# Performance work log

Measured on AMD Instinct MI355X. Metric: run time of the kernel, lower is better.

The kernel has to match this reference:

```python
import jax, jax.numpy as jnp
import numpy as np

ALPHABET = 8
DIM = 128
SEQ_LEN = 8192
POWER_ITERS = 200


def setup_inputs() -> dict:
    key = jax.random.key(0)
    k1, k2, k3 = jax.random.split(key, 3)
    return {
        "Kraus_op_re": jax.random.uniform(k1, (ALPHABET, DIM, DIM), dtype=jnp.float32),
        "Kraus_op_im": jax.random.uniform(k2, (ALPHABET, DIM, DIM), dtype=jnp.float32),
        "sequence": jax.random.randint(k3, (SEQ_LEN,), 0, ALPHABET),
    }


def _leading_eig(K):
    # K: [A, d, d] complex. Power iteration on the transfer map and its adjoint.
    d = K.shape[-1]
    Kc = K.conj()

    def body_r(rhor, _):
        # rhov = sum_x K_x @ rhor @ K_x^H
        rhov = jnp.einsum("aij,jk,alk->il", K, rhor, Kc)
        mu = jnp.trace(rhov).real
        return rhov / mu.astype(rhov.dtype), None

    rhor, _ = jax.lax.scan(body_r, jnp.eye(d, dtype=K.dtype) / d, None, length=POWER_ITERS)

    def body_l(carry, _):
        rhol, _ = carry
        # rhov = sum_x K_x^H @ rhol @ K_x
        rhov = jnp.einsum("aji,jk,akl->il", Kc, rhol, K)
        mu = jnp.trace(rhov).real
        return (rhov / mu.astype(rhov.dtype), mu), None

    (rhol, mu), _ = jax.lax.scan(
        body_l, (jnp.eye(d, dtype=K.dtype), jnp.asarray(1.0, jnp.float32)), None, length=POWER_ITERS
    )
    return rhor, rhol, mu


def reference(Kraus_op_re, Kraus_op_im, sequence):
    K = Kraus_op_re.astype(jnp.complex64) + 1j * Kraus_op_im.astype(jnp.complex64)
    rhor, rhol, lam = _leading_eig(K)
    # normalize so that trace(rho @ rhol) == 1
    rho0 = rhor / jnp.trace(rhor @ rhol).real.astype(rhor.dtype)
    Kn = K / jnp.sqrt(lam).astype(K.dtype)  # Kraus ops rescaled by sqrt(leading eigenvalue)
    L = sequence.shape[0]

    def step(carry, inp):
        rho, logp = carry
        i, x = inp
        Kx = Kn[x]
        rho = Kx @ rho @ Kx.conj().T
        px = jnp.where(i == L - 1, jnp.trace(rho @ rhol).real, jnp.trace(rho).real)
        logp = logp - jnp.log2(px)
        rho = rho / px.astype(rho.dtype)
        return (rho, logp), None

    (_, log_p), _ = jax.lax.scan(
        step, (rho0, jnp.asarray(0.0, jnp.float32)), (jnp.arange(L), sequence)
    )
    return log_p[None]  # matches torch.tensor([0.0]) accumulator shape (1,)
```

## Files before the change

### kernel.cpp

```cpp
#include <hip/hip_runtime.h>

typedef unsigned int u32;
typedef unsigned short u16;
typedef __attribute__((ext_vector_type(4))) float f32x4;
typedef __attribute__((ext_vector_type(8))) short s16x8;
typedef __attribute__((ext_vector_type(4))) u32 u32x4;

#define DIMN 128
#define MATN (DIMN*DIMN)
#define NA 8
#define LSEQ 8192
#define NTOK (LSEQ/2)
#define PITERS 4
#define S1SH 5
#define S2SH 6
#define CHSH 7
#define P2SH 8

struct WS {
  u16 *Kb, *P2b, *rho, *nodes0, *nodes1, *rootR, *rootI;
  int *tok, *E0, *E1, *Eroot;
  float *trbuf;
  float *out;
  int G, g;
};

__device__ __forceinline__ u16 f2bf(float x){
  u32 u = __float_as_uint(x);
  u32 r = (u + 0x7FFFu + ((u >> 16) & 1u)) >> 16;
  return (u16)r;
}
__device__ __forceinline__ float bf2f(u16 u){ return __uint_as_float(((u32)u) << 16); }
__device__ __forceinline__ u32 cvtpk(float lo, float hi){
  u32 r; asm("v_cvt_pk_bf16_f32 %0, %1, %2" : "=v"(r) : "v"(lo), "v"(hi)); return r;
}
__device__ __forceinline__ s16x8 negi(s16x8 v){
  return __builtin_bit_cast(s16x8, __builtin_bit_cast(u32x4, v) ^ 0x80008000u);
}
__device__ __forceinline__ int swz16(int maj, int b){
  return maj*256 + (((((b >> 4) + maj*5) & 15) << 4) | (b & 15));
}
__device__ __forceinline__ void cfma2(float2& c, float2 a, float2 b){
  c.x = fmaf(a.x, b.x, c.x); c.x = fmaf(-a.y, b.y, c.x);
  c.y = fmaf(a.x, b.y, c.y); c.y = fmaf(a.y, b.x, c.y);
}
template<int CA, int CB>
__device__ __forceinline__ void cmfma(s16x8 a_r, s16x8 a_i, s16x8 b_r, s16x8 b_i,
                                      f32x4& qr, f32x4& qi){
  s16x8 t1 = (CA ^ CB) ? a_i : negi(a_i);
  s16x8 t2 = CB ? negi(a_r) : a_r;
  s16x8 t3 = CA ? negi(a_i) : a_i;
  qr = __builtin_amdgcn_mfma_f32_16x16x32_bf16(a_r, b_r, qr, 0,0,0);
  qr = __builtin_amdgcn_mfma_f32_16x16x32_bf16(t1,  b_i, qr, 0,0,0);
  qi = __builtin_amdgcn_mfma_f32_16x16x32_bf16(t2,  b_i, qi, 0,0,0);
  qi = __builtin_amdgcn_mfma_f32_16x16x32_bf16(t3,  b_r, qi, 0,0,0);
}

__global__ __launch_bounds__(256) void k_init(const int* seq, WS w){
  int gid = blockIdx.x*256 + threadIdx.x;
  int gsz = gridDim.x*256;
  for (int i = gid; i < NTOK; i += gsz)
    w.tok[i] = seq[2*i+1]*NA + seq[2*i];
  for (int i = gid; i < 4*MATN; i += gsz){
    int plane = (i >> 14) & 1, rem = i & (MATN-1);
    u16 v = (plane == 0 && (rem >> 7) == (rem & 127)) ? f2bf(1.f) : (u16)0;
    w.rho[i] = v;
  }
  if (gid < 32) w.trbuf[gid] = 0.f;
}

__global__ __launch_bounds__(256) void k_kb(const float* Kre, const float* Kim, WS w){
  __shared__ u16 Lr[32][36], Li[32][36];
  int blk = blockIdx.x, x = blk >> 4, tile = blk & 15;
  int row0 = (tile>>2)*32, col0 = (tile&3)*32;
  int t = threadIdx.x;
  { int r = t>>3, cch = t&7;
    size_t off = (size_t)x*MATN + (size_t)(row0+r)*128 + col0 + cch*4;
    float4 vr = *(const float4*)(Kre + off);
    float4 vi = *(const float4*)(Kim + off);
    Lr[r][cch*4+0] = f2bf(vr.x); Lr[r][cch*4+1] = f2bf(vr.y);
    Lr[r][cch*4+2] = f2bf(vr.z); Lr[r][cch*4+3] = f2bf(vr.w);
    Li[r][cch*4+0] = f2bf(vi.x); Li[r][cch*4+1] = f2bf(vi.y);
    Li[r][cch*4+2] = f2bf(vi.z); Li[r][cch*4+3] = f2bf(vi.w);
  }
  __syncthreads();
  u16* b = w.Kb + (size_t)x*4*MATN;
  { int r = t>>3, cch = t&7;
    *(uint2*)&b[(row0+r)*128 + col0 + cch*4]        = *(uint2*)&Lr[r][cch*4];
    *(uint2*)&b[MATN + (row0+r)*128 + col0 + cch*4] = *(uint2*)&Li[r][cch*4];
  }
  { int c = t>>3, rch = t&7;
    ushort4 vr, vi;
    vr.x = Lr[rch*4+0][c]; vr.y = Lr[rch*4+1][c];
    vr.z = Lr[rch*4+2][c]; vr.w = Lr[rch*4+3][c];
    vi.x = Li[rch*4+0][c]; vi.y = Li[rch*4+1][c];
    vi.z = Li[rch*4+2][c]; vi.w = Li[rch*4+3][c];
    *(ushort4*)&b[2*MATN + (col0+c)*128 + row0 + rch*4] = vr;
    *(ushort4*)&b[3*MATN + (col0+c)*128 + row0 + rch*4] = vi;
  }
}

__global__ __launch_bounds__(256) void k_p2(const float* Kre, const float* Kim, WS w){
  __shared__ float2 As[16][33], Bs[16][33];
  int blk = blockIdx.x, mat = blk >> 4, tile = blk & 15;
  int a = mat >> 3, b = mat & 7;
  int row0 = (tile>>2)*32, col0 = (tile&3)*32;
  int t = threadIdx.x, ti = t & 15, tk = t >> 4;
  float2 acc[4] = {{0,0},{0,0},{0,0},{0,0}};
  for (int k0 = 0; k0 < 128; k0 += 16){
    { int r = t >> 4, kk = t & 15;
      size_t i0 = (size_t)a*MATN + (size_t)(row0+r)*DIMN + k0+kk;
      size_t i1 = i0 + 16*DIMN;
      As[kk][r]    = make_float2(Kre[i0], Kim[i0]);
      As[kk][r+16] = make_float2(Kre[i1], Kim[i1]); }
    { int kk = t >> 5, c = t & 31;
      size_t i0 = (size_t)b*MATN + (size_t)(k0+kk)*DIMN + col0+c;
      size_t i1 = i0 + 8*DIMN;
      Bs[kk][c]   = make_float2(Kre[i0], Kim[i0]);
      Bs[kk+8][c] = make_float2(Kre[i1], Kim[i1]); }
    __syncthreads();
    #pragma unroll
    for (int jj = 0; jj < 16; jj++){
      float2 a0 = As[jj][ti], a1 = As[jj][ti+16];
      float2 b0 = Bs[jj][tk], b1 = Bs[jj][tk+16];
      cfma2(acc[0], a0, b0); cfma2(acc[1], a0, b1);
      cfma2(acc[2], a1, b0); cfma2(acc[3], a1, b1);
    }
    __syncthreads();
  }
  u16* Lr = (u16*)As; u16* Li = (u16*)Bs;
  const float sc = 1.f/(1<<P2SH);
  Lr[ti*36+tk]         = f2bf(acc[0].x*sc); Li[ti*36+tk]         = f2bf(acc[0].y*sc);
  Lr[ti*36+tk+16]      = f2bf(acc[1].x*sc); Li[ti*36+tk+16]      = f2bf(acc[1].y*sc);
  Lr[(ti+16)*36+tk]    = f2bf(acc[2].x*sc); Li[(ti+16)*36+tk]    = f2bf(acc[2].y*sc);
  Lr[(ti+16)*36+tk+16] = f2bf(acc[3].x*sc); Li[(ti+16)*36+tk+16] = f2bf(acc[3].y*sc);
  __syncthreads();
  u16* base = w.P2b + (size_t)mat*4*MATN;
  { int r = t>>3, cch = t&7;
    *(uint2*)&base[(row0+r)*128 + col0 + cch*4]        = *(uint2*)&Lr[r*36 + cch*4];
    *(uint2*)&base[MATN + (row0+r)*128 + col0 + cch*4] = *(uint2*)&Li[r*36 + cch*4];
  }
  { int c = t>>3, rch = t&7;
    ushort4 vr, vi;
    vr.x = Lr[(rch*4+0)*36 + c]; vr.y = Lr[(rch*4+1)*36 + c];
    vr.z = Lr[(rch*4+2)*36 + c]; vr.w = Lr[(rch*4+3)*36 + c];
    vi.x = Li[(rch*4+0)*36 + c]; vi.y = Li[(rch*4+1)*36 + c];
    vi.z = Li[(rch*4+2)*36 + c]; vi.w = Li[(rch*4+3)*36 + c];
    *(ushort4*)&base[2*MATN + (col0+c)*128 + row0 + rch*4] = vr;
    *(ushort4*)&base[3*MATN + (col0+c)*128 + row0 + rch*4] = vi;
  }
}

__device__ __forceinline__ void ccompute(const u16* Ar, const u16* Ai,
    const char* Pr, const char* Pi, f32x4 (&qr)[2][4], f32x4 (&qi)[2][4], int t){
  int wv = t>>6, lane = t&63, l15 = lane&15, hi = lane>>4;
  int wr = (wv>>1)*32, wc = (wv&1)*64;
  #pragma unroll
  for (int m=0;m<2;m++)
    #pragma unroll
    for (int n=0;n<4;n++){ qr[m][n] = (f32x4){0,0,0,0}; qi[m][n] = (f32x4){0,0,0,0}; }
  #pragma unroll
  for (int kk = 0; kk < 4; kk++){
    int kb = kk*32 + hi*8;
    s16x8 a_r[2], a_i[2];
    #pragma unroll
    for (int m=0;m<2;m++){
      int r = wr + m*16 + l15;
      a_r[m] = *(const s16x8*)(Ar + r*128 + kb);
      a_i[m] = *(const s16x8*)(Ai + r*128 + kb);
    }
    #pragma unroll
    for (int n=0;n<4;n++){
      int c = wc + n*16 + l15;
      int o = swz16(c, kb*2);
      s16x8 b_r = *(const s16x8*)(Pr + o);
      s16x8 b_i = *(const s16x8*)(Pi + o);
      #pragma unroll
      for (int m=0;m<2;m++)
        cmfma<0,0>(a_r[m], a_i[m], b_r, b_i, qr[m][n], qi[m][n]);
    }
  }
}
__device__ __forceinline__ void pwrite8(char* Pr, char* Pi,
    f32x4 (&qr)[2][4], f32x4 (&qi)[2][4], float sc, int t){
  int wv = t>>6, lane = t&63, l15 = lane&15, hi = lane>>4;
  int wr = (wv>>1)*32, wc = (wv&1)*64;
  #pragma unroll
  for (int m=0;m<2;m++)
    #pragma unroll
    for (int n=0;n<4;n++){
      int c = wc + n*16 + l15, r0 = wr + m*16 + hi*4;
      uint2 pr, pi;
      pr.x = cvtpk(qr[m][n][0]*sc, qr[m][n][1]*sc);
      pr.y = cvtpk(qr[m][n][2]*sc, qr[m][n][3]*sc);
      pi.x = cvtpk(qi[m][n][0]*sc, qi[m][n][1]*sc);
      pi.y = cvtpk(qi[m][n][2]*sc, qi[m][n][3]*sc);
      int o = swz16(c, r0*2);
      *(uint2*)(Pr + o) = pr;
      *(uint2*)(Pi + o) = pi;
    }
}
__device__ __forceinline__ int renorm8(char* Pr, char* Pi,
    f32x4 (&qr)[2][4], f32x4 (&qi)[2][4], int t){
  int wv = t>>6, lane = t&63;
  float lm = 0.f;
  #pragma unroll
  for (int m=0;m<2;m++)
    #pragma unroll
    for (int n=0;n<4;n++)
      #pragma unroll
      for (int j=0;j<4;j++)
        lm = fmaxf(lm, fmaxf(fabsf(qr[m][n][j]), fabsf(qi[m][n][j])));
  #pragma unroll
  for (int o = 32; o > 0; o >>= 1) lm = fmaxf(lm, __shfl_xor(lm, o, 64));
  if (lane == 0) ((float*)Pr)[wv] = lm;
  __syncthreads();
  float mx = 0.f;
  #pragma unroll
  for (int i = 0; i < 8; i++) mx = fmaxf(mx, ((float*)Pr)[i]);
  int e = 0; if (mx > 0.f) frexpf(mx, &e);
  __syncthreads();
  pwrite8(Pr, Pi, qr, qi, ldexpf(1.f, -e), t);
  return e;
}
__device__ __forceinline__ void stage_cols(const u16* gr, const u16* gi,
                                           char* Pr, char* Pi, int t){
  #pragma unroll
  for (int i = 0; i < 4; i++){
    int chunk = t + i*512;
    int c = chunk >> 4, rr = chunk & 15;
    int o = swz16(c, rr*16);
    *(uint4*)(Pr + o) = *(const uint4*)(gr + c*128 + rr*8);
    *(uint4*)(Pi + o) = *(const uint4*)(gi + c*128 + rr*8);
  }
}
__device__ __forceinline__ void write_node(u16* dr, u16* di,
    const char* Pr, const char* Pi, bool rowLayout, int t){
  if (!rowLayout){
    #pragma unroll
    for (int i = 0; i < 4; i++){
      int chunk = t + i*512;
      int c = chunk >> 4, rr = chunk & 15;
      int o = swz16(c, rr*16);
      *(uint4*)(dr + c*128 + rr*8) = *(const uint4*)(Pr + o);
      *(uint4*)(di + c*128 + rr*8) = *(const uint4*)(Pi + o);
    }
  } else {
    for (int idx = t; idx < MATN; idx += 512){
      int r = idx >> 7, c = idx & 127;
      int o = swz16(c, r*2);
      dr[idx] = *(const u16*)(Pr + o);
      di[idx] = *(const u16*)(Pi + o);
    }
  }
}

__global__ __launch_bounds__(512,2) void k_chain(WS w){
  __shared__ __align__(16) char Pr[32768];
  __shared__ __align__(16) char Pi[32768];
  int p = blockIdx.x, t = threadIdx.x;
  int tok0 = w.tok[p*w.g];
  const u16* b0 = w.P2b + (size_t)tok0*4*MATN;
  stage_cols(b0 + 2*MATN, b0 + 3*MATN, Pr, Pi, t);
  f32x4 qr[2][4], qi[2][4];
  int eLast = 0;
  for (int s = 1; s < w.g; s++){
    const u16* tb = w.P2b + (size_t)w.tok[p*w.g + s]*4*MATN;
    __syncthreads();
    ccompute(tb, tb + MATN, Pr, Pi, qr, qi, t);
    __syncthreads();
    if (s < w.g-1) pwrite8(Pr, Pi, qr, qi, 1.f/(1<<CHSH), t);
    else eLast = renorm8(Pr, Pi, qr, qi, t);
  }
  __syncthreads();
  u16* slot = w.nodes0 + (size_t)p*2*MATN;
  write_node(slot, slot + MATN, Pr, Pi, (p & 3) != 0, t);
  if (t == 0) w.E0[p] = P2SH*w.g + CHSH*(w.g-2) + eLast;
}

__global__ __launch_bounds__(512,2) void k_level(WS w, int srcIs0, int radix,
                                                 int mask, int isRoot){
  __shared__ __align__(16) char Pr[32768];
  __shared__ __align__(16) char Pi[32768];
  int p = blockIdx.x, t = threadIdx.x;
  const u16* src = srcIs0 ? w.nodes0 : w.nodes1;
  u16* dst       = srcIs0 ? w.nodes1 : w.nodes0;
  const int* Es  = srcIs0 ? w.E0 : w.E1;
  int* Ed        = srcIs0 ? w.E1 : w.E0;
  const u16* B = src + (size_t)(radix*p)*2*MATN;
  stage_cols(B, B + MATN, Pr, Pi, t);
  int E = 0;
  for (int j = 0; j < radix; j++) E += Es[radix*p + j];
  f32x4 qr[2][4], qi[2][4];
  for (int j = 1; j < radix; j++){
    const u16* A = src + (size_t)(radix*p + j)*2*MATN;
    __syncthreads();
    ccompute(A, A + MATN, Pr, Pi, qr, qi, t);
    __syncthreads();
    E += renorm8(Pr, Pi, qr, qi, t);
  }
  __syncthreads();
  u16* slot = dst + (size_t)p*2*MATN;
  write_node(slot, slot + MATN, Pr, Pi, ((p & mask) != 0) || isRoot, t);
  if (t == 0) Ed[p] = E;
}

__global__ __launch_bounds__(512,1) void k_pow(WS w, int par){
  __shared__ __align__(16) char Rr[32768];
  __shared__ __align__(16) char Ri[32768];
  __shared__ __align__(16) char Yr[32768];
  __shared__ __align__(16) char Yi[32768];
  int b = blockIdx.x, side = b >> 3, rb = b & 7;
  int t = threadIdx.x, wv = t>>6, lane = t&63, l15 = lane&15, hi = lane>>4;
  const u16* rhoS = w.rho + (size_t)((par*2 + side)*2)*MATN;
  stage_cols(rhoS, rhoS + MATN, Rr, Ri, t);
  __syncthreads();
  {
    int x = wv;
    const u16* Ab = w.Kb + (size_t)(x*4 + (side ? 2 : 0))*MATN;
    const u16* Ar = Ab; const u16* Ai = Ab + MATN;
    f32x4 q1r[8], q1i[8];
    #pragma unroll
    for (int n=0;n<8;n++){ q1r[n] = (f32x4){0,0,0,0}; q1i[n] = (f32x4){0,0,0,0}; }
    #pragma unroll
    for (int kk = 0; kk < 4; kk++){
      int kb = kk*32 + hi*8;
      int r = rb*16 + l15;
      s16x8 a_r = *(const s16x8*)(Ar + r*128 + kb);
      s16x8 a_i = *(const s16x8*)(Ai + r*128 + kb);
      #pragma unroll
      for (int n=0;n<8;n++){
        int c = n*16 + l15;
        int o = swz16(c, kb*2);
        s16x8 b_r = *(const s16x8*)(Rr + o);
        s16x8 b_i = *(const s16x8*)(Ri + o);
        if (side == 0) cmfma<0,0>(a_r, a_i, b_r, b_i, q1r[n], q1i[n]);
        else           cmfma<1,0>(a_r, a_i, b_r, b_i, q1r[n], q1i[n]);
      }
    }
    const float sc = 1.f/(1<<S1SH);
    #pragma unroll
    for (int n=0;n<8;n++)
      #pragma unroll
      for (int q=0;q<4;q++){
        int lr = hi*4 + q, c = n*16 + l15;
        *(u16*)(Yr + x*4096 + swz16(lr, c*2)) = f2bf(q1r[n][q]*sc);
        *(u16*)(Yi + x*4096 + swz16(lr, c*2)) = f2bf(q1i[n][q]*sc);
      }
  }
  __syncthreads();
  {
    int c0 = wv*16, c = c0 + l15;
    f32x4 q2r = {0,0,0,0}, q2i = {0,0,0,0};
    #pragma unroll 2
    for (int x = 0; x < 8; x++){
      const u16* Bb = w.Kb + (size_t)(x*4 + (side ? 2 : 0))*MATN;
      const u16* Br = Bb; const u16* Bi = Bb + MATN;
      #pragma unroll
      for (int kk = 0; kk < 4; kk++){
        int kb = kk*32 + hi*8;
        s16x8 a_r = *(const s16x8*)(Yr + x*4096 + swz16(l15, kb*2));
        s16x8 a_i = *(const s16x8*)(Yi + x*4096 + swz16(l15, kb*2));
        s16x8 b_r = *(const s16x8*)(Br + c*128 + kb);
        s16x8 b_i = *(const s16x8*)(Bi + c*128 + kb);
        if (side == 0) cmfma<0,1>(a_r, a_i, b_r, b_i, q2r, q2i);
        else           cmfma<0,0>(a_r, a_i, b_r, b_i, q2r, q2i);
      }
    }
    const float sc = 1.f/(1<<S2SH);
    u16* Dr = w.rho + (size_t)(((par^1)*2 + side)*2)*MATN;
    u16* Di = Dr + MATN;
    int r0g = rb*16 + hi*4;
    uint2 pr, pi;
    pr.x = cvtpk(q2r[0]*sc, q2r[1]*sc); pr.y = cvtpk(q2r[2]*sc, q2r[3]*sc);
    pi.x = cvtpk(q2i[0]*sc, q2i[1]*sc); pi.y = cvtpk(q2i[2]*sc, q2i[3]*sc);
    *(uint2*)(Dr + c*128 + r0g) = pr;
    *(uint2*)(Di + c*128 + r0g) = pi;
    if (side == 1 && wv == rb){
      float tr = 0.f;
      #pragma unroll
      for (int q=0;q<4;q++) if (hi*4 + q == l15) tr += q2r[q]*sc;
      #pragma unroll
      for (int o = 32; o > 0; o >>= 1) tr += __shfl_xor(tr, o, 64);
      if (lane == 0) w.trbuf[par*16 + 8 + rb] = tr;
    }
  }
}

__global__ __launch_bounds__(512) void k_epi(WS w){
  __shared__ __align__(16) char T1r[32768];
  __shared__ __align__(16) char T1i[32768];
  int t = threadIdx.x, wv = t>>6, lane = t&63, l15 = lane&15, hi = lane>>4;
  int wr = (wv>>2)*64, wc = (wv&3)*32;
  f32x4 qr[4][2], qi[4][2];
  const u16* Ar = w.rho;
  const u16* Ai = Ar + MATN;
  #pragma unroll
  for (int m=0;m<4;m++)
    #pragma unroll
    for (int n=0;n<2;n++){ qr[m][n] = (f32x4){0,0,0,0}; qi[m][n] = (f32x4){0,0,0,0}; }
  #pragma unroll
  for (int kk = 0; kk < 4; kk++){
    int kb = kk*32 + hi*8;
    #pragma unroll
    for (int m=0;m<4;m++){
      int r = wr + m*16 + l15;
      s16x8 a_r = *(const s16x8*)(Ar + r*128 + kb);
      s16x8 a_i = *(const s16x8*)(Ai + r*128 + kb);
      #pragma unroll
      for (int n=0;n<2;n++){
        int c = wc + n*16 + l15;
        s16x8 b_r = *(const s16x8*)(w.rootR + c*128 + kb);
        s16x8 b_i = *(const s16x8*)(w.rootI + c*128 + kb);
        cmfma<0,0>(a_r, a_i, b_r, b_i, qr[m][n], qi[m][n]);
      }
    }
  }
  {
    const float sc = 1.f/(1<<CHSH);
    #pragma unroll
    for (int m=0;m<4;m++)
      #pragma unroll
      for (int n=0;n<2;n++){
        int c = wc + n*16 + l15, r0 = wr + m*16 + hi*4;
        uint2 pr, pi;
        pr.x = cvtpk(qr[m][n][0]*sc, qr[m][n][1]*sc);
        pr.y = cvtpk(qr[m][n][2]*sc, qr[m][n][3]*sc);
        pi.x = cvtpk(qi[m][n][0]*sc, qi[m][n][1]*sc);
        pi.y = cvtpk(qi[m][n][2]*sc, qi[m][n][3]*sc);
        int o = swz16(c, r0*2);
        *(uint2*)(T1r + o) = pr;
        *(uint2*)(T1i + o) = pi;
      }
  }
  __syncthreads();
  #pragma unroll
  for (int m=0;m<4;m++)
    #pragma unroll
    for (int n=0;n<2;n++){ qr[m][n] = (f32x4){0,0,0,0}; qi[m][n] = (f32x4){0,0,0,0}; }
  #pragma unroll
  for (int kk = 0; kk < 4; kk++){
    int kb = kk*32 + hi*8;
    #pragma unroll
    for (int m=0;m<4;m++){
      int r = wr + m*16 + l15;
      int o = swz16(r, kb*2);
      s16x8 a_r = *(const s16x8*)(T1r + o);
      s16x8 a_i = *(const s16x8*)(T1i + o);
      #pragma unroll
      for (int n=0;n<2;n++){
        int c = wc + n*16 + l15;
        s16x8 b_r = *(const s16x8*)(w.rootR + c*128 + kb);
        s16x8 b_i = *(const s16x8*)(w.rootI + c*128 + kb);
        cmfma<0,1>(a_r, a_i, b_r, b_i, qr[m][n], qi[m][n]);
      }
    }
  }
  __syncthreads();
  double* red = (double*)T1r;
  const u16* rlr = w.rho + (size_t)2*MATN;
  const u16* rli = rlr + MATN;
  double a1 = 0.0;
  #pragma unroll
  for (int m=0;m<4;m++)
    #pragma unroll
    for (int n=0;n<2;n++){
      int c = wc + n*16 + l15, r0 = wr + m*16 + hi*4;
      #pragma unroll
      for (int q=0;q<4;q++){
        int r = r0 + q;
        float lr = bf2f(rlr[r*128 + c]), li = bf2f(rli[r*128 + c]);
        a1 += (double)qr[m][n][q]*lr - (double)qi[m][n][q]*li;
      }
    }
  red[t] = a1; __syncthreads();
  for (int o = 256; o > 0; o >>= 1){ if (t < o) red[t] += red[t+o]; __syncthreads(); }
  double that = red[0]; __syncthreads();
  const u16* rrr = w.rho;
  const u16* rri = rrr + MATN;
  double a2 = 0.0;
  for (int idx = t; idx < MATN; idx += 512){
    int c = idx >> 7, r = idx & 127;
    float ar_ = bf2f(rrr[idx]), ai_ = bf2f(rri[idx]);
    float lr  = bf2f(rlr[r*128 + c]), li = bf2f(rli[r*128 + c]);
    a2 += (double)ar_*lr - (double)ai_*li;
  }
  red[t] = a2; __syncthreads();
  for (int o = 256; o > 0; o >>= 1){ if (t < o) red[t] += red[t+o]; __syncthreads(); }
  double trrl = red[0];
  if (t == 0){
    double T0 = 0.0, T1s = 0.0;
    for (int s = 0; s < 8; s++){ T0 += w.trbuf[8+s]; T1s += w.trbuf[16+8+s]; }
    double lam = ldexp(T1s / T0, S1SH + S2SH);
    double logp = (double)LSEQ * log2(lam) - 2.0*(double)w.Eroot[0] - (double)CHSH
                  - log2(fmax(that, 1e-300)) + log2(fmax(trrl, 1e-300));
    w.out[0] = (float)logp;
  }
}

static inline size_t aln256(size_t x){ return (x + 255) & ~(size_t)255; }

extern "C" void kernel_launch(void* const* d_in, const int* in_sizes, int n_in,
                              void* d_out, int out_size, void* d_ws, size_t ws_size,
                              hipStream_t stream){
  const float* Kre = (const float*)d_in[0];
  const float* Kim = (const float*)d_in[1];
  const int*   seq = (const int*)d_in[2];

  size_t fixedBytes = aln256((size_t)NA*4*MATN*2) + aln256((size_t)64*4*MATN*2)
                    + aln256((size_t)8*MATN*2) + aln256(NTOK*4)
                    + 2*aln256(512*4) + aln256(32*4);
  size_t need512 = fixedBytes + aln256((size_t)512*2*MATN*2) + aln256((size_t)128*2*MATN*2);
  int G = (ws_size >= need512) ? 512 : 256;
  int g = NTOK / G;

  WS w{};
  char* p = (char*)d_ws;
  auto take = [&](size_t bytes)->char*{ char* r = p; p += aln256(bytes); return r; };
  w.Kb    = (u16*)take((size_t)NA*4*MATN*2);
  w.P2b   = (u16*)take((size_t)64*4*MATN*2);
  w.rho   = (u16*)take((size_t)8*MATN*2);
  w.nodes0= (u16*)take((size_t)G*2*MATN*2);
  w.nodes1= (u16*)take((size_t)(G/4)*2*MATN*2);
  w.tok   = (int*)take(NTOK*4);
  w.E0    = (int*)take(512*4);
  w.E1    = (int*)take(512*4);
  w.trbuf = (float*)take(32*4);
  w.G = G; w.g = g;
  w.out = (float*)d_out;

  struct Lv { int blocks, srcIs0, radix, mask, isRoot; };
  Lv lv512[5] = { {128,1,4,3,0},{32,0,4,3,0},{8,1,4,3,0},{2,0,4,1,0},{1,1,2,0,1} };
  Lv lv256[4] = { {64,1,4,3,0},{16,0,4,3,0},{4,1,4,3,0},{1,0,4,0,1} };
  Lv* lv = (G == 512) ? lv512 : lv256;
  int nlv = (G == 512) ? 5 : 4;
  if (lv[nlv-1].srcIs0){ w.rootR = w.nodes1; w.Eroot = w.E1; }
  else                 { w.rootR = w.nodes0; w.Eroot = w.E0; }
  w.rootI = w.rootR + MATN;

  hipLaunchKernelGGL(k_init, dim3(64), dim3(256), 0, stream, seq, w);
  hipLaunchKernelGGL(k_kb, dim3(NA*16), dim3(256), 0, stream, Kre, Kim, w);
  hipLaunchKernelGGL(k_p2, dim3(64*16), dim3(256), 0, stream, Kre, Kim, w);
  hipLaunchKernelGGL(k_chain, dim3(G), dim3(512), 0, stream, w);
  for (int l = 0; l < nlv; l++)
    hipLaunchKernelGGL(k_level, dim3(lv[l].blocks), dim3(512), 0, stream, w,
                       lv[l].srcIs0, lv[l].radix, lv[l].mask, lv[l].isRoot);
  for (int k = 0; k < PITERS; k++)
    hipLaunchKernelGGL(k_pow, dim3(16), dim3(512), 0, stream, w, k & 1);
  hipLaunchKernelGGL(k_epi, dim3(1), dim3(512), 0, stream, w);
}
```

Baseline: 328.3 us.

## Double-buffer LDS in chain/level kernels, prefetch A operands into registers, fix grid

```diff
diff --git a/kernel.cpp b/kernel.cpp
--- a/kernel.cpp
+++ b/kernel.cpp
@@ -16,13 +16,14 @@
 #define S2SH 6
 #define CHSH 7
 #define P2SH 8
+#define GCH 256
+#define GLG 16
 
 struct WS {
   u16 *Kb, *P2b, *rho, *nodes0, *nodes1, *rootR, *rootI;
   int *tok, *E0, *E1, *Eroot;
   float *trbuf;
   float *out;
-  int G, g;
 };
 
 __device__ __forceinline__ u16 f2bf(float x){
@@ -56,20 +57,8 @@
   qi = __builtin_amdgcn_mfma_f32_16x16x32_bf16(t3,  b_r, qi, 0,0,0);
 }
 
-__global__ __launch_bounds__(256) void k_init(const int* seq, WS w){
-  int gid = blockIdx.x*256 + threadIdx.x;
-  int gsz = gridDim.x*256;
-  for (int i = gid; i < NTOK; i += gsz)
-    w.tok[i] = seq[2*i+1]*NA + seq[2*i];
-  for (int i = gid; i < 4*MATN; i += gsz){
-    int plane = (i >> 14) & 1, rem = i & (MATN-1);
-    u16 v = (plane == 0 && (rem >> 7) == (rem & 127)) ? f2bf(1.f) : (u16)0;
-    w.rho[i] = v;
-  }
-  if (gid < 32) w.trbuf[gid] = 0.f;
-}
-
-__global__ __launch_bounds__(256) void k_kb(const float* Kre, const float* Kim, WS w){
+__global__ __launch_bounds__(256) void k_kbinit(const float* Kre, const float* Kim,
+                                                const int* seq, WS w){
   __shared__ u16 Lr[32][36], Li[32][36];
   int blk = blockIdx.x, x = blk >> 4, tile = blk & 15;
   int row0 = (tile>>2)*32, col0 = (tile&3)*32;
@@ -98,6 +87,15 @@
     *(ushort4*)&b[2*MATN + (col0+c)*128 + row0 + rch*4] = vr;
     *(ushort4*)&b[3*MATN + (col0+c)*128 + row0 + rch*4] = vi;
   }
+  int gid = blockIdx.x*256 + t, gsz = gridDim.x*256;
+  for (int i = gid; i < NTOK; i += gsz)
+    w.tok[i] = seq[2*i+1]*NA + seq[2*i];
+  for (int i = gid; i < 4*MATN; i += gsz){
+    int plane = (i >> 14) & 1, rem = i & (MATN-1);
+    u16 v = (plane == 0 && (rem >> 7) == (rem & 127)) ? f2bf(1.f) : (u16)0;
+    w.rho[i] = v;
+  }
+  if (gid < 32) w.trbuf[gid] = 0.f;
 }
 
 __global__ __launch_bounds__(256) void k_p2(const float* Kre, const float* Kim, WS w){
@@ -151,24 +149,29 @@
   }
 }
 
-__device__ __forceinline__ void ccompute(const u16* Ar, const u16* Ai,
-    const char* Pr, const char* Pi, f32x4 (&qr)[2][4], f32x4 (&qi)[2][4], int t){
-  int wv = t>>6, lane = t&63, l15 = lane&15, hi = lane>>4;
-  int wr = (wv>>1)*32, wc = (wv&1)*64;
-  #pragma unroll
-  for (int m=0;m<2;m++)
-    #pragma unroll
-    for (int n=0;n<4;n++){ qr[m][n] = (f32x4){0,0,0,0}; qi[m][n] = (f32x4){0,0,0,0}; }
+__device__ __forceinline__ void loadA(const u16* Ar, const u16* Ai,
+    int wr, int l15, int hi, s16x8 (&fr)[4][2], s16x8 (&fi)[4][2]){
   #pragma unroll
   for (int kk = 0; kk < 4; kk++){
     int kb = kk*32 + hi*8;
-    s16x8 a_r[2], a_i[2];
-    #pragma unroll
-    for (int m=0;m<2;m++){
+    #pragma unroll
+    for (int m = 0; m < 2; m++){
       int r = wr + m*16 + l15;
-      a_r[m] = *(const s16x8*)(Ar + r*128 + kb);
-      a_i[m] = *(const s16x8*)(Ai + r*128 + kb);
-    }
+      fr[kk][m] = *(const s16x8*)(Ar + r*128 + kb);
+      fi[kk][m] = *(const s16x8*)(Ai + r*128 + kb);
+    }
+  }
+}
+__device__ __forceinline__ void ccomputeR(const s16x8 (&fr)[4][2], const s16x8 (&fi)[4][2],
+    const char* Pr, const char* Pi, f32x4 (&qr)[2][4], f32x4 (&qi)[2][4],
+    int wc, int l15, int hi){
+  #pragma unroll
+  for (int m=0;m<2;m++)
+    #pragma unroll
+    for (int n=0;n<4;n++){ qr[m][n] = (f32x4){0,0,0,0}; qi[m][n] = (f32x4){0,0,0,0}; }
+  #pragma unroll
+  for (int kk = 0; kk < 4; kk++){
+    int kb = kk*32 + hi*8;
     #pragma unroll
     for (int n=0;n<4;n++){
       int c = wc + n*16 + l15;
@@ -177,11 +180,11 @@
       s16x8 b_i = *(const s16x8*)(Pi + o);
       #pragma unroll
       for (int m=0;m<2;m++)
-        cmfma<0,0>(a_r[m], a_i[m], b_r, b_i, qr[m][n], qi[m][n]);
-    }
-  }
-}
-__device__ __forceinline__ void pwrite8(char* Pr, char* Pi,
+        cmfma<0,0>(fr[kk][m], fi[kk][m], b_r, b_i, qr[m][n], qi[m][n]);
+    }
+  }
+}
+__device__ __forceinline__ void pwrite16(char* Pr, char* Pi,
     f32x4 (&qr)[2][4], f32x4 (&qi)[2][4], float sc, int t){
   int wv = t>>6, lane = t&63, l15 = lane&15, hi = lane>>4;
   int wr = (wv>>1)*32, wc = (wv&1)*64;
@@ -200,7 +203,7 @@
       *(uint2*)(Pi + o) = pi;
     }
 }
-__device__ __forceinline__ int renorm8(char* Pr, char* Pi,
+__device__ __forceinline__ int renorm_to(char* Pr, char* Pi, float* red,
     f32x4 (&qr)[2][4], f32x4 (&qi)[2][4], int t){
   int wv = t>>6, lane = t&63;
   float lm = 0.f;
@@ -213,18 +216,17 @@
         lm = fmaxf(lm, fmaxf(fabsf(qr[m][n][j]), fabsf(qi[m][n][j])));
   #pragma unroll
   for (int o = 32; o > 0; o >>= 1) lm = fmaxf(lm, __shfl_xor(lm, o, 64));
-  if (lane == 0) ((float*)Pr)[wv] = lm;
+  if (lane == 0) red[wv] = lm;
   __syncthreads();
   float mx = 0.f;
   #pragma unroll
-  for (int i = 0; i < 8; i++) mx = fmaxf(mx, ((float*)Pr)[i]);
+  for (int i = 0; i < 8; i++) mx = fmaxf(mx, red[i]);
   int e = 0; if (mx > 0.f) frexpf(mx, &e);
-  __syncthreads();
-  pwrite8(Pr, Pi, qr, qi, ldexpf(1.f, -e), t);
+  pwrite16(Pr, Pi, qr, qi, ldexpf(1.f, -e), t);
   return e;
 }
-__device__ __forceinline__ void stage_cols(const u16* gr, const u16* gi,
-                                           char* Pr, char* Pi, int t){
+__device__ __forceinline__ void stage_cols16(const u16* gr, const u16* gi,
+                                             char* Pr, char* Pi, int t){
   #pragma unroll
   for (int i = 0; i < 4; i++){
     int chunk = t + i*512;
@@ -234,7 +236,7 @@
     *(uint4*)(Pi + o) = *(const uint4*)(gi + c*128 + rr*8);
   }
 }
-__device__ __forceinline__ void write_node(u16* dr, u16* di,
+__device__ __forceinline__ void write_node16(u16* dr, u16* di,
     const char* Pr, const char* Pi, bool rowLayout, int t){
   if (!rowLayout){
     #pragma unroll
@@ -255,53 +257,93 @@
   }
 }
 
-__global__ __launch_bounds__(512,2) void k_chain(WS w){
-  __shared__ __align__(16) char Pr[32768];
-  __shared__ __align__(16) char Pi[32768];
+__global__ __launch_bounds__(512,1) void k_chain(WS w){
+  __shared__ __align__(16) char P0r[32768];
+  __shared__ __align__(16) char P0i[32768];
+  __shared__ __align__(16) char P1r[32768];
+  __shared__ __align__(16) char P1i[32768];
+  __shared__ float red[8];
   int p = blockIdx.x, t = threadIdx.x;
-  int tok0 = w.tok[p*w.g];
+  int wv = t>>6, lane = t&63, l15 = lane&15, hi = lane>>4;
+  int wr = (wv>>1)*32, wc = (wv&1)*64;
+  char *PrC = P0r, *PiC = P0i, *PrN = P1r, *PiN = P1i;
+  int tok0 = w.tok[p*GLG];
   const u16* b0 = w.P2b + (size_t)tok0*4*MATN;
-  stage_cols(b0 + 2*MATN, b0 + 3*MATN, Pr, Pi, t);
+  stage_cols16(b0 + 2*MATN, b0 + 3*MATN, PrC, PiC, t);
+  s16x8 A1r[4][2], A1i[4][2], A2r[4][2], A2i[4][2];
+  { const u16* tb = w.P2b + (size_t)w.tok[p*GLG + 1]*4*MATN;
+    loadA(tb, tb + MATN, wr, l15, hi, A1r, A1i); }
   f32x4 qr[2][4], qi[2][4];
   int eLast = 0;
-  for (int s = 1; s < w.g; s++){
-    const u16* tb = w.P2b + (size_t)w.tok[p*w.g + s]*4*MATN;
+  __syncthreads();
+  #pragma unroll 1
+  for (int s = 1; s < GLG; s += 2){
+    if (s+1 < GLG){
+      const u16* tb = w.P2b + (size_t)w.tok[p*GLG + s+1]*4*MATN;
+      loadA(tb, tb + MATN, wr, l15, hi, A2r, A2i);
+    }
+    ccomputeR(A1r, A1i, PrC, PiC, qr, qi, wc, l15, hi);
+    if (s < GLG-1) pwrite16(PrN, PiN, qr, qi, 1.f/(1<<CHSH), t);
+    else eLast = renorm_to(PrN, PiN, red, qr, qi, t);
     __syncthreads();
-    ccompute(tb, tb + MATN, Pr, Pi, qr, qi, t);
-    __syncthreads();
-    if (s < w.g-1) pwrite8(Pr, Pi, qr, qi, 1.f/(1<<CHSH), t);
-    else eLast = renorm8(Pr, Pi, qr, qi, t);
-  }
-  __syncthreads();
+    { char* x = PrC; PrC = PrN; PrN = x; x = PiC; PiC = PiN; PiN = x; }
+    if (s+1 < GLG){
+      if (s+2 < GLG){
+        const u16* tb = w.P2b + (size_t)w.tok[p*GLG + s+2]*4*MATN;
+        loadA(tb, tb + MATN, wr, l15, hi, A1r, A1i);
+      }
+      ccomputeR(A2r, A2i, PrC, PiC, qr, qi, wc, l15, hi);
+      if (s+1 < GLG-1) pwrite16(PrN, PiN, qr, qi, 1.f/(1<<CHSH), t);
+      else eLast = renorm_to(PrN, PiN, red, qr, qi, t);
+      __syncthreads();
+      { char* x = PrC; PrC = PrN; PrN = x; x = PiC; PiC = PiN; PiN = x; }
+    }
+  }
   u16* slot = w.nodes0 + (size_t)p*2*MATN;
-  write_node(slot, slot + MATN, Pr, Pi, (p & 3) != 0, t);
-  if (t == 0) w.E0[p] = P2SH*w.g + CHSH*(w.g-2) + eLast;
-}
-
-__global__ __launch_bounds__(512,2) void k_level(WS w, int srcIs0, int radix,
-                                                 int mask, int isRoot){
-  __shared__ __align__(16) char Pr[32768];
-  __shared__ __align__(16) char Pi[32768];
+  write_node16(slot, slot + MATN, PrC, PiC, (p & 3) != 0, t);
+  if (t == 0) w.E0[p] = P2SH*GLG + CHSH*(GLG-2) + eLast;
+}
+
+__global__ __launch_bounds__(512,1) void k_level(WS w, int srcIs0, int isRoot){
+  __shared__ __align__(16) char P0r[32768];
+  __shared__ __align__(16) char P0i[32768];
+  __shared__ __align__(16) char P1r[32768];
+  __shared__ __align__(16) char P1i[32768];
+  __shared__ float red[8];
   int p = blockIdx.x, t = threadIdx.x;
+  int wv = t>>6, lane = t&63, l15 = lane&15, hi = lane>>4;
+  int wr = (wv>>1)*32, wc = (wv&1)*64;
+  char *PrC = P0r, *PiC = P0i, *PrN = P1r, *PiN = P1i;
   const u16* src = srcIs0 ? w.nodes0 : w.nodes1;
   u16* dst       = srcIs0 ? w.nodes1 : w.nodes0;
   const int* Es  = srcIs0 ? w.E0 : w.E1;
   int* Ed        = srcIs0 ? w.E1 : w.E0;
-  const u16* B = src + (size_t)(radix*p)*2*MATN;
-  stage_cols(B, B + MATN, Pr, Pi, t);
-  int E = 0;
-  for (int j = 0; j < radix; j++) E += Es[radix*p + j];
+  const u16* B = src + (size_t)(4*p)*2*MATN;
+  stage_cols16(B, B + MATN, PrC, PiC, t);
+  s16x8 A1r[4][2], A1i[4][2], A2r[4][2], A2i[4][2];
+  { const u16* A = src + (size_t)(4*p+1)*2*MATN;
+    loadA(A, A + MATN, wr, l15, hi, A1r, A1i); }
+  int E = Es[4*p] + Es[4*p+1] + Es[4*p+2] + Es[4*p+3];
   f32x4 qr[2][4], qi[2][4];
-  for (int j = 1; j < radix; j++){
-    const u16* A = src + (size_t)(radix*p + j)*2*MATN;
-    __syncthreads();
-    ccompute(A, A + MATN, Pr, Pi, qr, qi, t);
-    __syncthreads();
-    E += renorm8(Pr, Pi, qr, qi, t);
-  }
-  __syncthreads();
+  __syncthreads();
+  { const u16* A = src + (size_t)(4*p+2)*2*MATN;
+    loadA(A, A + MATN, wr, l15, hi, A2r, A2i); }
+  ccomputeR(A1r, A1i, PrC, PiC, qr, qi, wc, l15, hi);
+  E += renorm_to(PrN, PiN, red, qr, qi, t);
+  __syncthreads();
+  { char* x = PrC; PrC = PrN; PrN = x; x = PiC; PiC = PiN; PiN = x; }
+  { const u16* A = src + (size_t)(4*p+3)*2*MATN;
+    loadA(A, A + MATN, wr, l15, hi, A1r, A1i); }
+  ccomputeR(A2r, A2i, PrC, PiC, qr, qi, wc, l15, hi);
+  E += renorm_to(PrN, PiN, red, qr, qi, t);
+  __syncthreads();
+  { char* x = PrC; PrC = PrN; PrN = x; x = PiC; PiC = PiN; PiN = x; }
+  ccomputeR(A1r, A1i, PrC, PiC, qr, qi, wc, l15, hi);
+  E += renorm_to(PrN, PiN, red, qr, qi, t);
+  __syncthreads();
+  { char* x = PrC; PrC = PrN; PrN = x; x = PiC; PiC = PiN; PiN = x; }
   u16* slot = dst + (size_t)p*2*MATN;
-  write_node(slot, slot + MATN, Pr, Pi, ((p & mask) != 0) || isRoot, t);
+  write_node16(slot, slot + MATN, PrC, PiC, ((p & 3) != 0) || isRoot, t);
   if (t == 0) Ed[p] = E;
 }
 
@@ -313,10 +355,9 @@
   int b = blockIdx.x, side = b >> 3, rb = b & 7;
   int t = threadIdx.x, wv = t>>6, lane = t&63, l15 = lane&15, hi = lane>>4;
   const u16* rhoS = w.rho + (size_t)((par*2 + side)*2)*MATN;
-  stage_cols(rhoS, rhoS + MATN, Rr, Ri, t);
-  __syncthreads();
-  {
-    int x = wv;
+  stage_cols16(rhoS, rhoS + MATN, Rr, Ri, t);
+  __syncthreads();
+  { int x = wv;
     const u16* Ab = w.Kb + (size_t)(x*4 + (side ? 2 : 0))*MATN;
     const u16* Ar = Ab; const u16* Ai = Ab + MATN;
     f32x4 q1r[8], q1i[8];
@@ -349,8 +390,7 @@
       }
   }
   __syncthreads();
-  {
-    int c0 = wv*16, c = c0 + l15;
+  { int c0 = wv*16, c = c0 + l15;
     f32x4 q2r = {0,0,0,0}, q2i = {0,0,0,0};
     #pragma unroll 2
     for (int x = 0; x < 8; x++){
@@ -507,44 +547,29 @@
   const float* Kim = (const float*)d_in[1];
   const int*   seq = (const int*)d_in[2];
 
-  size_t fixedBytes = aln256((size_t)NA*4*MATN*2) + aln256((size_t)64*4*MATN*2)
-                    + aln256((size_t)8*MATN*2) + aln256(NTOK*4)
-                    + 2*aln256(512*4) + aln256(32*4);
-  size_t need512 = fixedBytes + aln256((size_t)512*2*MATN*2) + aln256((size_t)128*2*MATN*2);
-  int G = (ws_size >= need512) ? 512 : 256;
-  int g = NTOK / G;
-
   WS w{};
   char* p = (char*)d_ws;
   auto take = [&](size_t bytes)->char*{ char* r = p; p += aln256(bytes); return r; };
   w.Kb    = (u16*)take((size_t)NA*4*MATN*2);
   w.P2b   = (u16*)take((size_t)64*4*MATN*2);
   w.rho   = (u16*)take((size_t)8*MATN*2);
-  w.nodes0= (u16*)take((size_t)G*2*MATN*2);
-  w.nodes1= (u16*)take((size_t)(G/4)*2*MATN*2);
+  w.nodes0= (u16*)take((size_t)GCH*2*MATN*2);
+  w.nodes1= (u16*)take((size_t)(GCH/4)*2*MATN*2);
   w.tok   = (int*)take(NTOK*4);
-  w.E0    = (int*)take(512*4);
-  w.E1    = (int*)take(512*4);
+  w.E0    = (int*)take(GCH*4);
+  w.E1    = (int*)take(GCH*4);
   w.trbuf = (float*)take(32*4);
-  w.G = G; w.g = g;
   w.out = (float*)d_out;
-
-  struct Lv { int blocks, srcIs0, radix, mask, isRoot; };
-  Lv lv512[5] = { {128,1,4,3,0},{32,0,4,3,0},{8,1,4,3,0},{2,0,4,1,0},{1,1,2,0,1} };
-  Lv lv256[4] = { {64,1,4,3,0},{16,0,4,3,0},{4,1,4,3,0},{1,0,4,0,1} };
-  Lv* lv = (G == 512) ? lv512 : lv256;
-  int nlv = (G == 512) ? 5 : 4;
-  if (lv[nlv-1].srcIs0){ w.rootR = w.nodes1; w.Eroot = w.E1; }
-  else                 { w.rootR = w.nodes0; w.Eroot = w.E0; }
-  w.rootI = w.rootR + MATN;
-
-  hipLaunchKernelGGL(k_init, dim3(64), dim3(256), 0, stream, seq, w);
-  hipLaunchKernelGGL(k_kb, dim3(NA*16), dim3(256), 0, stream, Kre, Kim, w);
+  w.rootR = w.nodes0; w.rootI = w.nodes0 + MATN;
+  w.Eroot = w.E0;
+
+  hipLaunchKernelGGL(k_kbinit, dim3(NA*16), dim3(256), 0, stream, Kre, Kim, seq, w);
   hipLaunchKernelGGL(k_p2, dim3(64*16), dim3(256), 0, stream, Kre, Kim, w);
-  hipLaunchKernelGGL(k_chain, dim3(G), dim3(512), 0, stream, w);
-  for (int l = 0; l < nlv; l++)
-    hipLaunchKernelGGL(k_level, dim3(lv[l].blocks), dim3(512), 0, stream, w,
-                       lv[l].srcIs0, lv[l].radix, lv[l].mask, lv[l].isRoot);
+  hipLaunchKernelGGL(k_chain, dim3(GCH), dim3(512), 0, stream, w);
+  hipLaunchKernelGGL(k_level, dim3(64), dim3(512), 0, stream, w, 1, 0);
+  hipLaunchKernelGGL(k_level, dim3(16), dim3(512), 0, stream, w, 0, 0);
+  hipLaunchKernelGGL(k_level, dim3(4),  dim3(512), 0, stream, w, 1, 0);
+  hipLaunchKernelGGL(k_level, dim3(1),  dim3(512), 0, stream, w, 0, 1);
   for (int k = 0; k < PITERS; k++)
     hipLaunchKernelGGL(k_pow, dim3(16), dim3(512), 0, stream, w, k & 1);
   hipLaunchKernelGGL(k_epi, dim3(1), dim3(512), 0, stream, w);
```

New measurement: 347.9 us. +5.9%, slower.
